# Performance work log

Measured on AMD Instinct MI355X. Metric: run time of the kernel, lower is better.

## Reference

```python
import jax, jax.numpy as jnp
import numpy as np

B, CIN, COUT = 4, 32, 32
D1, D2, D3 = 64, 64, 64
M1, M2, M3 = 32, 32, 17  # n_modes with last dim -> 32//2+1 after rfft redundancy
INIT_STD = (2.0 / (CIN + COUT)) ** 0.5


def setup_inputs() -> dict:
    key = jax.random.key(0)
    k_x, k_wr, k_wi, k_b = jax.random.split(key, 4)
    x = jax.random.normal(k_x, (B, CIN, D1, D2, D3), dtype=jnp.float32)
    # ComplexDense factorized weight, normal_(0, init_std) on real and imag parts
    w_real = INIT_STD * jax.random.normal(k_wr, (CIN, COUT, M1, M2, M3), dtype=jnp.float32)
    w_imag = INIT_STD * jax.random.normal(k_wi, (CIN, COUT, M1, M2, M3), dtype=jnp.float32)
    # bias: (n_layers=1, out_channels, 1, 1, 1); we take index 0 slice
    bias = INIT_STD * jax.random.normal(k_b, (1, COUT, 1, 1, 1), dtype=jnp.float32)
    return {"x": x, "w_real": w_real, "w_imag": w_imag, "bias": bias}


def reference(x, w_real, w_imag, bias):
    fft_axes = (-3, -2, -1)
    b, cin, d1, d2, d3 = x.shape
    f3 = d3 // 2 + 1
    # forward rFFT, shift all but last (real) axis so low modes are centered
    xf = jnp.fft.rfftn(x, axes=fft_axes)               # (B, Cin, D1, D2, f3) complex
    xf = jnp.fft.fftshift(xf, axes=fft_axes[:-1])
    weight = w_real + 1j * w_imag                       # (Cin, Cout, M1, M2, M3)
    m1, m2, m3 = weight.shape[2:]
    s1, s2 = (d1 - m1) // 2, (d2 - m2) // 2
    xs = xf[:, :, s1:s1 + m1, s2:s2 + m2, :m3]          # centered low modes
    # channel contraction in Fourier space: abcde,bfcde->afcde
    out_modes = jnp.einsum('abcde,bfcde->afcde', xs, weight)
    out_fft = jnp.zeros((b, weight.shape[1], d1, d2, f3), dtype=out_modes.dtype)
    out_fft = out_fft.at[:, :, s1:s1 + m1, s2:s2 + m2, :m3].set(out_modes)
    # torch applies fftshift (not ifftshift); identical for even sizes
    out_fft = jnp.fft.fftshift(out_fft, axes=fft_axes[:-1])
    out = jnp.fft.irfftn(out_fft, s=(d1, d2, d3), axes=fft_axes)
    return out + bias[0]
```

## Files before the change

kernel.cpp:

```cpp
#include <hip/hip_runtime.h>
#include <math.h>

static constexpr int NB  = 4;
static constexpr int NC  = 32;

__device__ __attribute__((aligned(256))) float T3F[64 * 48];
__device__ __attribute__((aligned(256))) float2 T3I2[17 * 64];
__device__ __attribute__((aligned(256))) float T12F[64 * 64];
__device__ __attribute__((aligned(256))) float TINV[32 * 128];

__global__ __launch_bounds__(256) void k0_init() {
    const int t = blockIdx.x * 256 + threadIdx.x;
    if (t < 64 * 17) {
        int n = t / 17, k = t % 17;
        int idx = (n * k) & 63;
        float s, c;
        sincospif(idx / 32.0f, &s, &c);
        T3F[n * 48 + 2 * k] = c;  T3F[n * 48 + 2 * k + 1] = -s;
    }
    if (t < 64) {
        for (int q = 34; q < 48; ++q) T3F[t * 48 + q] = 0.f;
    }
    if (t < 17 * 64) {
        int k = t >> 6, n = t & 63;
        int idx = (n * k) & 63;
        float s, c;
        sincospif(idx / 32.0f, &s, &c);
        T3I2[t] = make_float2(c, s);
    }
    if (t < 64 * 32) {
        int n = t / 32, p = t % 32;
        int o = (p + 48) & 63;
        int idx = (o * n) & 63;
        float s, c;
        sincospif(idx / 32.0f, &s, &c);
        T12F[n * 64 + 2 * p] = c;  T12F[n * 64 + 2 * p + 1] = -s;
    }
    if (t < 32 * 64) {
        int p = t / 64, n = t % 64;
        int o = (p + 48) & 63;
        int idx = (o * n) & 63;
        float s, c;
        sincospif(idx / 32.0f, &s, &c);
        TINV[p * 128 + 2 * n] = c;  TINV[p * 128 + 2 * n + 1] = s;
    }
}

__device__ __forceinline__ void cmadd(float2& a, float2 x, float wx, float wy) {
    a.x = fmaf(x.x, wx, fmaf(-x.y, wy, a.x));
    a.y = fmaf(x.x, wy, fmaf( x.y, wx, a.y));
}

__global__ __launch_bounds__(64)
void k1_rfft_d3(const float* __restrict__ x, float2* __restrict__ o1) {
    __shared__ float tile[64 * 65];
    const int t = threadIdx.x, bid = blockIdx.x;
    const float4* src4 = (const float4*)(x + (size_t)bid * 4096);
    for (int j = 0; j < 16; ++j) {
        int f4 = j * 64 + t;
        float4 v = src4[f4];
        int d2 = f4 >> 4, n0 = (f4 & 15) << 2;
        float* p = &tile[d2 * 65 + n0];
        p[0] = v.x; p[1] = v.y; p[2] = v.z; p[3] = v.w;
    }
    __syncthreads();
    float ar[17], ai[17];
#pragma unroll
    for (int k = 0; k < 17; ++k) { ar[k] = 0.f; ai[k] = 0.f; }
    const float* row = &tile[t * 65];
    for (int n = 0; n < 64; ++n) {
        float xv = row[n];
        const float* w = &T3F[n * 48];
#pragma unroll
        for (int k = 0; k < 17; ++k) {
            ar[k] = fmaf(xv, w[2 * k], ar[k]);
            ai[k] = fmaf(xv, w[2 * k + 1], ai[k]);
        }
    }
    const int bc = bid >> 6, d1 = bid & 63;
    float2* dst = o1 + (size_t)bc * (17 * 4096) + d1 * 64 + t;
#pragma unroll
    for (int k = 0; k < 17; ++k)
        dst[(size_t)k * 4096] = make_float2(ar[k], ai[k]);
}

__global__ __launch_bounds__(256)
void k2a_dft_d2(const float2* __restrict__ in, float2* __restrict__ T) {
    __shared__ float smem[8320];
    float* re = smem;
    float* im = smem + 64 * 65;
    const int t = threadIdx.x;
    const size_t base = (size_t)blockIdx.x * 4096;
    for (int j = 0; j < 16; ++j) {
        int idx = j * 256 + t;
        float2 v = in[base + idx];
        int d1 = idx >> 6, n2 = idx & 63;
        re[d1 * 65 + n2] = v.x;
        im[d1 * 65 + n2] = v.y;
    }
    __syncthreads();
    const int d1 = t & 63;
    const int pg = __builtin_amdgcn_readfirstlane(t >> 6);
    float2 acc[8];
#pragma unroll
    for (int j = 0; j < 8; ++j) acc[j] = make_float2(0.f, 0.f);
    const float* rrow = &re[d1 * 65];
    const float* irow = &im[d1 * 65];
#pragma unroll 2
    for (int n2 = 0; n2 < 64; ++n2) {
        float xr = rrow[n2], xi = irow[n2];
        const float* w = &T12F[n2 * 64 + pg * 16];
#pragma unroll
        for (int j = 0; j < 8; ++j)
            cmadd(acc[j], make_float2(xr, xi), w[2 * j], w[2 * j + 1]);
    }
    __syncthreads();
    float2* tile = (float2*)smem;
#pragma unroll
    for (int j = 0; j < 8; ++j) tile[d1 * 33 + pg * 8 + j] = acc[j];
    __syncthreads();
    float2* dst = T + (size_t)blockIdx.x * 2048;
#pragma unroll
    for (int q = 0; q < 8; ++q) {
        int e = t * 8 + q;
        dst[e] = tile[(e >> 5) * 33 + (e & 31)];
    }
}

__global__ __launch_bounds__(544)
void k2b_dft_d1(const float2* __restrict__ T, float2* __restrict__ Y) {
    const int u = threadIdx.x;
    const int bc = blockIdx.x, pg = blockIdx.y;
    const int k3 = u % 17, p2 = u / 17;
    const float2* src = T + ((size_t)bc * 17 + k3) * 2048 + p2;
    float2 acc[8];
#pragma unroll
    for (int j = 0; j < 8; ++j) acc[j] = make_float2(0.f, 0.f);
#pragma unroll 2
    for (int n1 = 0; n1 < 64; ++n1) {
        float2 xv = src[n1 * 32];
        const float* w = &T12F[n1 * 64 + pg * 16];
#pragma unroll
        for (int j = 0; j < 8; ++j)
            cmadd(acc[j], xv, w[2 * j], w[2 * j + 1]);
    }
    float2* dst = Y + (size_t)bc * 17408 + (size_t)pg * 8 * 544 + u;
#pragma unroll
    for (int j = 0; j < 8; ++j) dst[(size_t)j * 544] = acc[j];
}

__global__ __launch_bounds__(64)
void k3_mix(const float2* __restrict__ Y, const float* __restrict__ wr,
            const float* __restrict__ wi, float2* __restrict__ Z) {
    const int m = blockIdx.x * 64 + threadIdx.x;
    const int ch = blockIdx.y;
    float2 acc[4][4];
#pragma unroll
    for (int a = 0; a < 4; ++a)
#pragma unroll
        for (int co = 0; co < 4; ++co) acc[a][co] = make_float2(0.f, 0.f);
#pragma unroll 8
    for (int cin = 0; cin < 32; ++cin) {
        float2 xv[4];
#pragma unroll
        for (int a = 0; a < 4; ++a)
            xv[a] = Y[((size_t)a * 32 + cin) * 17408 + m];
        size_t wb = ((size_t)cin * 32 + ch * 4) * 17408 + m;
#pragma unroll
        for (int co = 0; co < 4; ++co) {
            float wrv = wr[wb + (size_t)co * 17408];
            float wiv = wi[wb + (size_t)co * 17408];
#pragma unroll
            for (int a = 0; a < 4; ++a)
                cmadd(acc[a][co], xv[a], wrv, wiv);
        }
    }
#pragma unroll
    for (int a = 0; a < 4; ++a)
#pragma unroll
        for (int co = 0; co < 4; ++co)
            Z[((size_t)a * 32 + ch * 4 + co) * 17408 + m] = acc[a][co];
}

__global__ __launch_bounds__(544)
void k4a_idft_d1(const float2* __restrict__ Z, float2* __restrict__ U) {
    const int u = threadIdx.x;
    const int bf = blockIdx.x, ng = blockIdx.y;
    const float2* src = Z + (size_t)bf * 17408 + u;
    float2 acc[8];
#pragma unroll
    for (int j = 0; j < 8; ++j) acc[j] = make_float2(0.f, 0.f);
#pragma unroll 2
    for (int p1 = 0; p1 < 32; ++p1) {
        float2 xv = src[(size_t)p1 * 544];
        const float* w = &TINV[p1 * 128 + ng * 16];
#pragma unroll
        for (int j = 0; j < 8; ++j)
            cmadd(acc[j], xv, w[2 * j], w[2 * j + 1]);
    }
    float2* dst = U + (size_t)bf * 34816 + (size_t)ng * 8 * 544 + u;
#pragma unroll
    for (int j = 0; j < 8; ++j) dst[(size_t)j * 544] = acc[j];
}

__global__ __launch_bounds__(256)
void k45_ifft23(const float2* __restrict__ U, const float* __restrict__ bias,
                float* __restrict__ out) {
    __shared__ __align__(16) float2 Ur[32 * 18];
    __shared__ float2 W2[17 * 64];
    const int t = threadIdx.x;
    const int bf = blockIdx.x, n1 = blockIdx.y;
    const float2* src = U + (size_t)bf * 34816 + (size_t)n1 * 544;
    for (int j = t; j < 544; j += 256) {
        int p2 = j / 17, k3 = j - p2 * 17;
        Ur[p2 * 18 + k3] = src[j];
    }
    const int lane = t & 63;
    const int w = __builtin_amdgcn_readfirstlane(t >> 6);
    float2 tws[32];
#pragma unroll
    for (int p = 0; p < 32; ++p)
        tws[p] = *(const float2*)&TINV[p * 128 + 2 * lane];
    __syncthreads();
    const float inv2 = 2.0f / 262144.0f;
    {
        const int kb = w * 4;
        float A[4] = {0,0,0,0}, Bm[4] = {0,0,0,0};
        float C[4] = {0,0,0,0}, Dm[4] = {0,0,0,0};
#pragma unroll
        for (int p2 = 0; p2 < 32; ++p2) {
            float4 xa = *(const float4*)&Ur[p2 * 18 + kb];
            float4 xb = *(const float4*)&Ur[p2 * 18 + kb + 2];
            float c = tws[p2].x, s = tws[p2].y;
            A[0] = fmaf(xa.x, c, A[0]);  Bm[0] = fmaf(xa.y, s, Bm[0]);
            C[0] = fmaf(xa.x, s, C[0]);  Dm[0] = fmaf(xa.y, c, Dm[0]);
            A[1] = fmaf(xa.z, c, A[1]);  Bm[1] = fmaf(xa.w, s, Bm[1]);
            C[1] = fmaf(xa.z, s, C[1]);  Dm[1] = fmaf(xa.w, c, Dm[1]);
            A[2] = fmaf(xb.x, c, A[2]);  Bm[2] = fmaf(xb.y, s, Bm[2]);
            C[2] = fmaf(xb.x, s, C[2]);  Dm[2] = fmaf(xb.y, c, Dm[2]);
            A[3] = fmaf(xb.z, c, A[3]);  Bm[3] = fmaf(xb.w, s, Bm[3]);
            C[3] = fmaf(xb.z, s, C[3]);  Dm[3] = fmaf(xb.w, c, Dm[3]);
        }
#pragma unroll
        for (int j = 0; j < 4; ++j)
            W2[(kb + j) * 64 + lane] =
                make_float2((A[j] - Bm[j]) * inv2, (C[j] + Dm[j]) * inv2);
        if (w == 3) {
            float a = 0.f, b = 0.f, c2 = 0.f, d = 0.f;
#pragma unroll
            for (int p2 = 0; p2 < 32; ++p2) {
                float2 xv = Ur[p2 * 18 + 16];
                float c = tws[p2].x, s = tws[p2].y;
                a  = fmaf(xv.x, c, a);   b = fmaf(xv.y, s, b);
                c2 = fmaf(xv.x, s, c2);  d = fmaf(xv.y, c, d);
            }
            W2[16 * 64 + lane] = make_float2((a - b) * inv2, (c2 + d) * inv2);
        }
    }
    __syncthreads();
    float2 X[17];
#pragma unroll
    for (int k = 0; k < 17; ++k) X[k] = W2[k * 64 + lane];
    const float bv = bias[bf & 31];
    float y[16];
#pragma unroll
    for (int r = 0; r < 16; ++r) y[r] = fmaf(X[0].x, 0.5f, bv);
#pragma unroll
    for (int k = 1; k < 17; ++k) {
        const float2* tr = &T3I2[k * 64 + w * 16];
#pragma unroll
        for (int r = 0; r < 16; ++r) {
            float2 tw = tr[r];
            y[r] = fmaf(X[k].x, tw.x, y[r]);
            y[r] = fmaf(-X[k].y, tw.y, y[r]);
        }
    }
    float* dst = out + (size_t)bf * 262144 + (size_t)n1 * 4096
               + (size_t)lane * 64 + w * 16;
#pragma unroll
    for (int q = 0; q < 4; ++q)
        *(float4*)&dst[q * 4] =
            make_float4(y[q * 4], y[q * 4 + 1], y[q * 4 + 2], y[q * 4 + 3]);
}

extern "C" void kernel_launch(void* const* d_in, const int* in_sizes, int n_in,
                              void* d_out, int out_size, void* d_ws, size_t ws_size,
                              hipStream_t stream) {
    const float* x    = (const float*)d_in[0];
    const float* wr   = (const float*)d_in[1];
    const float* wi   = (const float*)d_in[2];
    const float* bias = (const float*)d_in[3];
    float* out = (float*)d_out;

    float2* A = (float2*)d_ws;
    float2* B = A + (size_t)2176 * 4096;
    float2* Y = A;
    float2* Z = A + (size_t)17825792 / 8;

    k0_init    <<<8, 256, 0, stream>>>();
    k1_rfft_d3 <<<NB * NC * 64, 64, 0, stream>>>(x, A);
    k2a_dft_d2 <<<2176, 256, 0, stream>>>(A, B);
    k2b_dft_d1 <<<dim3(128, 4), 544, 0, stream>>>(B, Y);
    k3_mix     <<<dim3(272, 8), 64, 0, stream>>>(Y, wr, wi, Z);
    k4a_idft_d1<<<dim3(128, 8), 544, 0, stream>>>(Z, B);
    k45_ifft23 <<<dim3(128, 64), 256, 0, stream>>>(B, bias, out);
}
```

Measured before the change: 307.7 us.

## Coalesce k2b reads via LDS transpose and batch four rows per k45 block

In k2b the thread-to-(k3,p2) mapping now puts p2 on the fast index, so the global reads of T are contiguous. Results are transposed through shared memory to keep the stores to Y coalesced. k45 now processes four n1 rows per block, reusing the per-lane twiddle registers and the bias across rows. It reads U directly from global memory instead of staging it in shared memory, which gives strided, non-vector loads and adds two barriers per row. It also has a quarter as many blocks.

Result: slower. 603.9 us (+96.3%).

```diff
diff --git a/kernel.cpp b/kernel.cpp
--- a/kernel.cpp
+++ b/kernel.cpp
@@ -129,9 +129,10 @@
 
 __global__ __launch_bounds__(544)
 void k2b_dft_d1(const float2* __restrict__ T, float2* __restrict__ Y) {
+    __shared__ float2 tile[8 * 544];
     const int u = threadIdx.x;
     const int bc = blockIdx.x, pg = blockIdx.y;
-    const int k3 = u % 17, p2 = u / 17;
+    const int k3 = u >> 5, p2 = u & 31;
     const float2* src = T + ((size_t)bc * 17 + k3) * 2048 + p2;
     float2 acc[8];
 #pragma unroll
@@ -144,9 +145,14 @@
         for (int j = 0; j < 8; ++j)
             cmadd(acc[j], xv, w[2 * j], w[2 * j + 1]);
     }
-    float2* dst = Y + (size_t)bc * 17408 + (size_t)pg * 8 * 544 + u;
-#pragma unroll
-    for (int j = 0; j < 8; ++j) dst[(size_t)j * 544] = acc[j];
+#pragma unroll
+    for (int j = 0; j < 8; ++j)
+        tile[j * 544 + p2 * 17 + k3] = acc[j];
+    __syncthreads();
+    float2* dst = Y + (size_t)bc * 17408 + (size_t)pg * 8 * 544;
+#pragma unroll
+    for (int i = 0; i < 8; ++i)
+        dst[u + i * 544] = tile[u + i * 544];
 }
 
 __global__ __launch_bounds__(64)
@@ -206,81 +212,75 @@
 __global__ __launch_bounds__(256)
 void k45_ifft23(const float2* __restrict__ U, const float* __restrict__ bias,
                 float* __restrict__ out) {
-    __shared__ __align__(16) float2 Ur[32 * 18];
     __shared__ float2 W2[17 * 64];
     const int t = threadIdx.x;
-    const int bf = blockIdx.x, n1 = blockIdx.y;
-    const float2* src = U + (size_t)bf * 34816 + (size_t)n1 * 544;
-    for (int j = t; j < 544; j += 256) {
-        int p2 = j / 17, k3 = j - p2 * 17;
-        Ur[p2 * 18 + k3] = src[j];
-    }
     const int lane = t & 63;
     const int w = __builtin_amdgcn_readfirstlane(t >> 6);
+    const int bf = blockIdx.x;
+    const int n1base = blockIdx.y * 4;
     float2 tws[32];
 #pragma unroll
     for (int p = 0; p < 32; ++p)
         tws[p] = *(const float2*)&TINV[p * 128 + 2 * lane];
-    __syncthreads();
+    const float bv = bias[bf & 31];
     const float inv2 = 2.0f / 262144.0f;
-    {
-        const int kb = w * 4;
+    const int kb = w * 4;
+    for (int p = 0; p < 4; ++p) {
+        const int n1 = n1base + p;
+        const float* srow = (const float*)(U + (size_t)bf * 34816 + (size_t)n1 * 544);
         float A[4] = {0,0,0,0}, Bm[4] = {0,0,0,0};
         float C[4] = {0,0,0,0}, Dm[4] = {0,0,0,0};
+        float ta = 0.f, tb = 0.f, tc = 0.f, td = 0.f;
 #pragma unroll
         for (int p2 = 0; p2 < 32; ++p2) {
-            float4 xa = *(const float4*)&Ur[p2 * 18 + kb];
-            float4 xb = *(const float4*)&Ur[p2 * 18 + kb + 2];
+            const float* sp = srow + (p2 * 17 + kb) * 2;
             float c = tws[p2].x, s = tws[p2].y;
-            A[0] = fmaf(xa.x, c, A[0]);  Bm[0] = fmaf(xa.y, s, Bm[0]);
-            C[0] = fmaf(xa.x, s, C[0]);  Dm[0] = fmaf(xa.y, c, Dm[0]);
-            A[1] = fmaf(xa.z, c, A[1]);  Bm[1] = fmaf(xa.w, s, Bm[1]);
-            C[1] = fmaf(xa.z, s, C[1]);  Dm[1] = fmaf(xa.w, c, Dm[1]);
-            A[2] = fmaf(xb.x, c, A[2]);  Bm[2] = fmaf(xb.y, s, Bm[2]);
-            C[2] = fmaf(xb.x, s, C[2]);  Dm[2] = fmaf(xb.y, c, Dm[2]);
-            A[3] = fmaf(xb.z, c, A[3]);  Bm[3] = fmaf(xb.w, s, Bm[3]);
-            C[3] = fmaf(xb.z, s, C[3]);  Dm[3] = fmaf(xb.w, c, Dm[3]);
+            A[0] = fmaf(sp[0], c, A[0]);  Bm[0] = fmaf(sp[1], s, Bm[0]);
+            C[0] = fmaf(sp[0], s, C[0]);  Dm[0] = fmaf(sp[1], c, Dm[0]);
+            A[1] = fmaf(sp[2], c, A[1]);  Bm[1] = fmaf(sp[3], s, Bm[1]);
+            C[1] = fmaf(sp[2], s, C[1]);  Dm[1] = fmaf(sp[3], c, Dm[1]);
+            A[2] = fmaf(sp[4], c, A[2]);  Bm[2] = fmaf(sp[5], s, Bm[2]);
+            C[2] = fmaf(sp[4], s, C[2]);  Dm[2] = fmaf(sp[5], c, Dm[2]);
+            A[3] = fmaf(sp[6], c, A[3]);  Bm[3] = fmaf(sp[7], s, Bm[3]);
+            C[3] = fmaf(sp[6], s, C[3]);  Dm[3] = fmaf(sp[7], c, Dm[3]);
+            if (w == 3) {
+                float xtr = srow[(p2 * 17 + 16) * 2];
+                float xti = srow[(p2 * 17 + 16) * 2 + 1];
+                ta = fmaf(xtr, c, ta);  tb = fmaf(xti, s, tb);
+                tc = fmaf(xtr, s, tc);  td = fmaf(xti, c, td);
+            }
         }
 #pragma unroll
         for (int j = 0; j < 4; ++j)
             W2[(kb + j) * 64 + lane] =
                 make_float2((A[j] - Bm[j]) * inv2, (C[j] + Dm[j]) * inv2);
-        if (w == 3) {
-            float a = 0.f, b = 0.f, c2 = 0.f, d = 0.f;
-#pragma unroll
-            for (int p2 = 0; p2 < 32; ++p2) {
-                float2 xv = Ur[p2 * 18 + 16];
-                float c = tws[p2].x, s = tws[p2].y;
-                a  = fmaf(xv.x, c, a);   b = fmaf(xv.y, s, b);
-                c2 = fmaf(xv.x, s, c2);  d = fmaf(xv.y, c, d);
+        if (w == 3)
+            W2[16 * 64 + lane] = make_float2((ta - tb) * inv2, (tc + td) * inv2);
+        __syncthreads();
+        float2 X[17];
+#pragma unroll
+        for (int k = 0; k < 17; ++k) X[k] = W2[k * 64 + lane];
+        __syncthreads();
+        float y[16];
+#pragma unroll
+        for (int r = 0; r < 16; ++r) y[r] = fmaf(X[0].x, 0.5f, bv);
+#pragma unroll
+        for (int k = 1; k < 17; ++k) {
+            const float2* tr = &T3I2[k * 64 + w * 16];
+#pragma unroll
+            for (int r = 0; r < 16; ++r) {
+                float2 tw = tr[r];
+                y[r] = fmaf(X[k].x, tw.x, y[r]);
+                y[r] = fmaf(-X[k].y, tw.y, y[r]);
             }
-            W2[16 * 64 + lane] = make_float2((a - b) * inv2, (c2 + d) * inv2);
         }
-    }
-    __syncthreads();
-    float2 X[17];
-#pragma unroll
-    for (int k = 0; k < 17; ++k) X[k] = W2[k * 64 + lane];
-    const float bv = bias[bf & 31];
-    float y[16];
-#pragma unroll
-    for (int r = 0; r < 16; ++r) y[r] = fmaf(X[0].x, 0.5f, bv);
-#pragma unroll
-    for (int k = 1; k < 17; ++k) {
-        const float2* tr = &T3I2[k * 64 + w * 16];
-#pragma unroll
-        for (int r = 0; r < 16; ++r) {
-            float2 tw = tr[r];
-            y[r] = fmaf(X[k].x, tw.x, y[r]);
-            y[r] = fmaf(-X[k].y, tw.y, y[r]);
-        }
-    }
-    float* dst = out + (size_t)bf * 262144 + (size_t)n1 * 4096
-               + (size_t)lane * 64 + w * 16;
-#pragma unroll
-    for (int q = 0; q < 4; ++q)
-        *(float4*)&dst[q * 4] =
-            make_float4(y[q * 4], y[q * 4 + 1], y[q * 4 + 2], y[q * 4 + 3]);
+        float* dst = out + (size_t)bf * 262144 + (size_t)n1 * 4096
+                   + (size_t)lane * 64 + w * 16;
+#pragma unroll
+        for (int q = 0; q < 4; ++q)
+            *(float4*)&dst[q * 4] =
+                make_float4(y[q * 4], y[q * 4 + 1], y[q * 4 + 2], y[q * 4 + 3]);
+    }
 }
 
 extern "C" void kernel_launch(void* const* d_in, const int* in_sizes, int n_in,
@@ -303,5 +303,5 @@
     k2b_dft_d1 <<<dim3(128, 4), 544, 0, stream>>>(B, Y);
     k3_mix     <<<dim3(272, 8), 64, 0, stream>>>(Y, wr, wi, Z);
     k4a_idft_d1<<<dim3(128, 8), 544, 0, stream>>>(Z, B);
-    k45_ifft23 <<<dim3(128, 64), 256, 0, stream>>>(B, bias, out);
-}
+    k45_ifft23 <<<dim3(128, 16), 256, 0, stream>>>(B, bias, out);
+}
```
